# Optimization experiments

Measured on AMD Instinct MI355X. Metric: run time of the kernel, lower is better.

## Reference

```python
import jax, jax.numpy as jnp
import numpy as np

S = 7          # grid size
B = 2          # boxes per cell
C = 20         # classes (last dim = B*5 + C = 30)
IMG = 448.0    # img_size
GAMMA_COORD = 5.0
GAMMA_NOOBJ = 0.5
BS = 8192


def setup_inputs() -> dict:
    key = jax.random.key(0)
    k1, k2, k3 = jax.random.split(key, 3)
    output = jax.random.uniform(k1, (BS, S, S, B * 5 + C), dtype=jnp.float32)
    target = jax.random.uniform(k2, (BS, S, S, B * 5 + C), dtype=jnp.float32)
    grid_mask_obj = jax.random.randint(k3, (BS, S, S), 0, 2).astype(jnp.int32)
    return {"output": output, "target": target, "grid_mask_obj": grid_mask_obj}


def _decode_xyxy(t):
    """t: (bs,S,S,B*5) raw boxes -> pixel-space corner boxes x1,y1,x2,y2, each (bs,S,S,B)."""
    boxes = t.reshape(t.shape[:3] + (B, 5))
    cell = 1.0 / S
    gx = (jnp.arange(S, dtype=t.dtype) * cell)[None, None, :, None]  # varies along m (col)
    gy = (jnp.arange(S, dtype=t.dtype) * cell)[None, :, None, None]  # varies along n (row)
    x = (boxes[..., 0] * cell + gx) * IMG
    y = (boxes[..., 1] * cell + gy) * IMG
    w = boxes[..., 2] * IMG
    h = boxes[..., 3] * IMG
    return x - w / 2, y - h / 2, x + w / 2, y + h / 2


def _yolo_loss(output, target, grid_mask_obj):
    bs = output.shape[0]
    obj = (grid_mask_obj != 0).astype(output.dtype)          # (bs,S,S)

    boxes_o = output[..., : B * 5].reshape(output.shape[:3] + (B, 5))
    boxes_t = target[..., : B * 5].reshape(target.shape[:3] + (B, 5))

    # --- IoU of each predicted box vs target box 0 (matches box_iou(...)[:, 0]) ---
    ox1, oy1, ox2, oy2 = _decode_xyxy(output[..., : B * 5])   # (bs,S,S,B)
    tx1, ty1, tx2, ty2 = _decode_xyxy(target[..., : B * 5])
    tx1, ty1, tx2, ty2 = tx1[..., :1], ty1[..., :1], tx2[..., :1], ty2[..., :1]  # target box 0
    iw = jnp.clip(jnp.minimum(ox2, tx2) - jnp.maximum(ox1, tx1), 0.0)
    ih = jnp.clip(jnp.minimum(oy2, ty2) - jnp.maximum(oy1, ty1), 0.0)
    inter = iw * ih
    area_o = (ox2 - ox1) * (oy2 - oy1)
    area_t = (tx2 - tx1) * (ty2 - ty1)
    ious = inter / (area_o + area_t - inter)                  # (bs,S,S,B)

    max_iou = jnp.max(ious, axis=-1)                          # (bs,S,S)
    max_id = jnp.argmax(ious, axis=-1)                        # (bs,S,S)
    onehot = jax.nn.one_hot(max_id, B, dtype=output.dtype)
    obj_ij_mask = onehot * obj[..., None]
    obj_ij_ious = onehot * max_iou[..., None] * obj[..., None]

    box_id_reg = jnp.argmax(obj_ij_mask, axis=-1)             # (bs,S,S)
    box_id_conf = jnp.argmax(obj_ij_ious, axis=-1)

    sel_o = jnp.take_along_axis(boxes_o, box_id_reg[..., None, None], axis=3)[..., 0, :]
    sel_t = jnp.take_along_axis(boxes_t, box_id_reg[..., None, None], axis=3)[..., 0, :]
    xy_loss = jnp.sum(obj * jnp.sum((sel_o[..., 0:2] - sel_t[..., 0:2]) ** 2, axis=-1))
    wh_loss = jnp.sum(obj * jnp.sum((jnp.sqrt(sel_o[..., 2:4]) - jnp.sqrt(sel_t[..., 2:4])) ** 2, axis=-1))

    # --- confidence loss (obj cells): predicted conf vs matched IoU ---
    conf_o = boxes_o[..., 4]                                  # (bs,S,S,B)
    conf_t = boxes_t[..., 4]
    sel_c = jnp.take_along_axis(conf_o, box_id_conf[..., None], axis=3)[..., 0]
    sel_iou = jnp.take_along_axis(obj_ij_ious, box_id_conf[..., None], axis=3)[..., 0]
    c_loss_obj = jnp.sum(obj * (sel_c - sel_iou) ** 2)

    # --- confidence loss (noobj cells): all B boxes ---
    c_loss_noobj = jnp.sum((1.0 - obj)[..., None] * (conf_o - conf_t) ** 2)

    # --- class probability loss (obj cells) ---
    cls_loss = jnp.sum(obj[..., None] * (output[..., B * 5:] - target[..., B * 5:]) ** 2)

    return (GAMMA_COORD * (xy_loss + wh_loss)
            + c_loss_obj
            + GAMMA_NOOBJ * c_loss_noobj
            + cls_loss) / bs


def reference(output, target, grid_mask_obj):
    return _yolo_loss(output, target, grid_mask_obj)
```

## Files before the change

### kernel.cpp

```cpp
#include <hip/hip_runtime.h>


constexpr float CELLW_  = 1.0f / 7.0f;
constexpr float IMG_    = 448.0f;
constexpr float INV_BS_ = 1.0f / 8192.0f;
constexpr int   NCELL_  = 8192 * 7 * 7;
constexpr int   NBLK_   = NCELL_ / 256;

__global__ __launch_bounds__(256) void yolo_partial_kernel(
    const float* __restrict__ outp, const float* __restrict__ tgtp,
    const int* __restrict__ maskp, float* __restrict__ partial)
{
    __shared__ int   lmask[256];
    __shared__ float lo[256 * 11];
    __shared__ float lt[256 * 11];

    const int tid   = threadIdx.x;
    const int cell0 = blockIdx.x * 256;

    lmask[tid] = maskp[cell0 + tid];
    __syncthreads();

    const float2* po = reinterpret_cast<const float2*>(outp) + (size_t)cell0 * 15;
    const float2* pt = reinterpret_cast<const float2*>(tgtp) + (size_t)cell0 * 15;

    float acc = 0.0f;

    int c  = (2 * tid) / 30;
    int ch = (2 * tid) - c * 30;

#pragma unroll
    for (int k = 0; k < 15; ++k) {
        const int j = tid + 256 * k;
        float2 vo = po[j];
        float2 vt = pt[j];
        if (ch < 10) {
            lo[c * 11 + ch]     = vo.x;
            lo[c * 11 + ch + 1] = vo.y;
            lt[c * 11 + ch]     = vt.x;
            lt[c * 11 + ch + 1] = vt.y;
        } else {
            float dx = vo.x - vt.x;
            float dy = vo.y - vt.y;
            acc += lmask[c] ? (dx * dx + dy * dy) : 0.0f;
        }
        ch += 2; c += 17;
        if (ch >= 30) { ch -= 30; c += 1; }
    }
    __syncthreads();

    {
        const float* o = &lo[tid * 11];
        const float* t = &lt[tid * 11];
        const int    m = lmask[tid];

        const int rem = (cell0 + tid) % 49;
        const float gx = (float)(rem % 7) * CELLW_;
        const float gy = (float)(rem / 7) * CELLW_;

        const float tx = (t[0] * CELLW_ + gx) * IMG_;
        const float ty = (t[1] * CELLW_ + gy) * IMG_;
        const float tw = t[2] * IMG_, th = t[3] * IMG_;
        const float tx1 = tx - tw * 0.5f, tx2 = tx + tw * 0.5f;
        const float ty1 = ty - th * 0.5f, ty2 = ty + th * 0.5f;
        const float area_t = (tx2 - tx1) * (ty2 - ty1);

        float iou[2];
#pragma unroll
        for (int b = 0; b < 2; ++b) {
            float b0 = (b == 0) ? o[0] : o[5];
            float b1 = (b == 0) ? o[1] : o[6];
            float b2 = (b == 0) ? o[2] : o[7];
            float b3 = (b == 0) ? o[3] : o[8];
            float x = (b0 * CELLW_ + gx) * IMG_;
            float y = (b1 * CELLW_ + gy) * IMG_;
            float w = b2 * IMG_, h = b3 * IMG_;
            float x1 = x - w * 0.5f, x2 = x + w * 0.5f;
            float y1 = y - h * 0.5f, y2 = y + h * 0.5f;
            float iw = fmaxf(fminf(x2, tx2) - fmaxf(x1, tx1), 0.0f);
            float ih = fmaxf(fminf(y2, ty2) - fmaxf(y1, ty1), 0.0f);
            float inter = iw * ih;
            float area_o = (x2 - x1) * (y2 - y1);
            iou[b] = inter / (area_o + area_t - inter);
        }

        const int   max_id  = (iou[1] > iou[0]) ? 1 : 0;
        const float max_iou = fmaxf(iou[0], iou[1]);

        const float so0 = max_id ? o[5] : o[0];
        const float so1 = max_id ? o[6] : o[1];
        const float so2 = max_id ? o[7] : o[2];
        const float so3 = max_id ? o[8] : o[3];
        const float st0 = max_id ? t[5] : t[0];
        const float st1 = max_id ? t[6] : t[1];
        const float st2 = max_id ? t[7] : t[2];
        const float st3 = max_id ? t[8] : t[3];

        const float dxy0 = so0 - st0, dxy1 = so1 - st1;
        const float xy_loss = dxy0 * dxy0 + dxy1 * dxy1;

        const float dwh0 = sqrtf(so2) - sqrtf(st2);
        const float dwh1 = sqrtf(so3) - sqrtf(st3);
        const float wh_loss = dwh0 * dwh0 + dwh1 * dwh1;

        const int   id_conf = (max_iou > 0.0f) ? max_id : 0;
        const float sel_c   = id_conf ? o[9] : o[4];
        const float sel_iou = (id_conf == max_id) ? max_iou : 0.0f;
        const float dcf     = sel_c - sel_iou;
        const float c_obj   = dcf * dcf;

        const float dn0 = o[4] - t[4], dn1 = o[9] - t[9];
        const float c_noobj = dn0 * dn0 + dn1 * dn1;

        acc += m ? (5.0f * (xy_loss + wh_loss) + c_obj)
                 : (0.5f * c_noobj);
    }

#pragma unroll
    for (int off = 32; off > 0; off >>= 1)
        acc += __shfl_down(acc, off);

    __shared__ float wsum[4];
    const int lane = threadIdx.x & 63;
    const int wid  = threadIdx.x >> 6;
    if (lane == 0) wsum[wid] = acc;
    __syncthreads();
    if (threadIdx.x == 0)
        partial[blockIdx.x] = wsum[0] + wsum[1] + wsum[2] + wsum[3];
}

__global__ __launch_bounds__(256) void yolo_reduce_kernel(
    const float* __restrict__ partial, float* __restrict__ out)
{
    float a = 0.0f;
    for (int i = threadIdx.x; i < NBLK_; i += 256)
        a += partial[i];

#pragma unroll
    for (int off = 32; off > 0; off >>= 1)
        a += __shfl_down(a, off);

    __shared__ float wsum[4];
    const int lane = threadIdx.x & 63;
    const int wid  = threadIdx.x >> 6;
    if (lane == 0) wsum[wid] = a;
    __syncthreads();
    if (threadIdx.x == 0)
        out[0] = (wsum[0] + wsum[1] + wsum[2] + wsum[3]) * INV_BS_;
}

extern "C" void kernel_launch(void* const* d_in, const int* in_sizes, int n_in,
                              void* d_out, int out_size, void* d_ws, size_t ws_size,
                              hipStream_t stream) {
    const float* outp = (const float*)d_in[0];
    const float* tgtp = (const float*)d_in[1];
    const int*   mask = (const int*)d_in[2];
    float*       res  = (float*)d_out;
    float*       part = (float*)d_ws;

    const int ncell = in_sizes[2];
    const int blocks = ncell / 256;

    yolo_partial_kernel<<<blocks, 256, 0, stream>>>(outp, tgtp, mask, part);
    yolo_reduce_kernel<<<1, 256, 0, stream>>>(part, res);
}
```

Measured before the change: 122.4 us.

## Stream inputs as float4 grid-stride pass and gather box fields only for object cells

Replaces the shared-memory staging with a persistent grid-stride loop over float4 elements. Each element is weighted by its channel type and mask, which covers the class loss and the noobj confidence loss. A second pass per cell re-reads the first ten box fields from global memory only for object cells to compute IoU and the coordinate and confidence losses. This removes LDS traffic and barriers and uses a fixed 2048-block grid, at the cost of extra mask loads and partly uncoalesced re-reads of box data, which should mostly hit cache.

```diff
diff --git a/kernel.cpp b/kernel.cpp
--- a/kernel.cpp
+++ b/kernel.cpp
@@ -1,119 +1,127 @@
 #include <hip/hip_runtime.h>
 
 
+constexpr int   NCELL_  = 8192 * 7 * 7;
+constexpr int   NF4_    = NCELL_ * 30 / 4;
+constexpr int   TPB_    = 256;
+constexpr int   NBLK_   = 2048;
+constexpr int   NTH_    = TPB_ * NBLK_;
 constexpr float CELLW_  = 1.0f / 7.0f;
 constexpr float IMG_    = 448.0f;
 constexpr float INV_BS_ = 1.0f / 8192.0f;
-constexpr int   NCELL_  = 8192 * 7 * 7;
-constexpr int   NBLK_   = NCELL_ / 256;
 
-__global__ __launch_bounds__(256) void yolo_partial_kernel(
+__global__ __launch_bounds__(TPB_) void yolo_partial_kernel(
     const float* __restrict__ outp, const float* __restrict__ tgtp,
     const int* __restrict__ maskp, float* __restrict__ partial)
 {
-    __shared__ int   lmask[256];
-    __shared__ float lo[256 * 11];
-    __shared__ float lt[256 * 11];
-
-    const int tid   = threadIdx.x;
-    const int cell0 = blockIdx.x * 256;
-
-    lmask[tid] = maskp[cell0 + tid];
-    __syncthreads();
-
-    const float2* po = reinterpret_cast<const float2*>(outp) + (size_t)cell0 * 15;
-    const float2* pt = reinterpret_cast<const float2*>(tgtp) + (size_t)cell0 * 15;
-
+    const int gtid = blockIdx.x * TPB_ + threadIdx.x;
     float acc = 0.0f;
 
-    int c  = (2 * tid) / 30;
-    int ch = (2 * tid) - c * 30;
+    {
+        const float4* o4p = reinterpret_cast<const float4*>(outp);
+        const float4* t4p = reinterpret_cast<const float4*>(tgtp);
+
+        unsigned D    = 4u * (unsigned)gtid;
+        unsigned cell = D / 30u;
+        int      ch   = (int)(D - cell * 30u);
+
+        for (int i = gtid; i < NF4_; i += NTH_) {
+            float4 o4 = o4p[i];
+            float4 t4 = t4p[i];
+            int m0 = maskp[cell];
+            int m1 = maskp[(ch == 28) ? cell + 1u : cell];
+            float mf0 = m0 ? 1.0f : 0.0f;
+            float mf1 = m1 ? 1.0f : 0.0f;
 
 #pragma unroll
-    for (int k = 0; k < 15; ++k) {
-        const int j = tid + 256 * k;
-        float2 vo = po[j];
-        float2 vt = pt[j];
-        if (ch < 10) {
-            lo[c * 11 + ch]     = vo.x;
-            lo[c * 11 + ch + 1] = vo.y;
-            lt[c * 11 + ch]     = vt.x;
-            lt[c * 11 + ch + 1] = vt.y;
-        } else {
-            float dx = vo.x - vt.x;
-            float dy = vo.y - vt.y;
-            acc += lmask[c] ? (dx * dx + dy * dy) : 0.0f;
+            for (int j = 0; j < 4; ++j) {
+                int   chj   = ch + j;
+                bool  cross = (chj >= 30);
+                int   chv   = cross ? chj - 30 : chj;
+                float mf    = cross ? mf1 : mf0;
+                float w = (chv >= 10) ? mf
+                        : ((chv == 4) | (chv == 9)) ? 0.5f * (1.0f - mf)
+                        : 0.0f;
+                float ov = (j == 0) ? o4.x : (j == 1) ? o4.y : (j == 2) ? o4.z : o4.w;
+                float tv = (j == 0) ? t4.x : (j == 1) ? t4.y : (j == 2) ? t4.z : t4.w;
+                float d = ov - tv;
+                acc += w * d * d;
+            }
+
+            cell += 69905u; ch += 2;
+            if (ch >= 30) { ch -= 30; cell += 1u; }
         }
-        ch += 2; c += 17;
-        if (ch >= 30) { ch -= 30; c += 1; }
     }
-    __syncthreads();
 
-    {
-        const float* o = &lo[tid * 11];
-        const float* t = &lt[tid * 11];
-        const int    m = lmask[tid];
+    if (gtid < NCELL_) {
+        const int c = gtid;
+        const int m = maskp[c];
+        if (m) {
+            const float2* po = reinterpret_cast<const float2*>(outp) + (size_t)c * 15;
+            const float2* pt = reinterpret_cast<const float2*>(tgtp) + (size_t)c * 15;
+            float2 a0 = po[0], a1 = po[1], a2 = po[2], a3 = po[3], a4 = po[4];
+            float2 b0 = pt[0], b1 = pt[1], b2 = pt[2], b3 = pt[3], b4 = pt[4];
+            const float o0 = a0.x, o1 = a0.y, o2 = a1.x, o3 = a1.y, o4v = a2.x;
+            const float o5 = a2.y, o6 = a3.x, o7 = a3.y, o8 = a4.x, o9 = a4.y;
+            const float t0 = b0.x, t1 = b0.y, t2 = b1.x, t3 = b1.y;
+            const float t5 = b2.y, t6 = b3.x, t7 = b3.y, t8 = b4.x;
 
-        const int rem = (cell0 + tid) % 49;
-        const float gx = (float)(rem % 7) * CELLW_;
-        const float gy = (float)(rem / 7) * CELLW_;
+            const int rem = c % 49;
+            const float gx = (float)(rem % 7) * CELLW_;
+            const float gy = (float)(rem / 7) * CELLW_;
 
-        const float tx = (t[0] * CELLW_ + gx) * IMG_;
-        const float ty = (t[1] * CELLW_ + gy) * IMG_;
-        const float tw = t[2] * IMG_, th = t[3] * IMG_;
-        const float tx1 = tx - tw * 0.5f, tx2 = tx + tw * 0.5f;
-        const float ty1 = ty - th * 0.5f, ty2 = ty + th * 0.5f;
-        const float area_t = (tx2 - tx1) * (ty2 - ty1);
+            const float tx = (t0 * CELLW_ + gx) * IMG_;
+            const float ty = (t1 * CELLW_ + gy) * IMG_;
+            const float tw = t2 * IMG_, th = t3 * IMG_;
+            const float tx1 = tx - tw * 0.5f, tx2 = tx + tw * 0.5f;
+            const float ty1 = ty - th * 0.5f, ty2 = ty + th * 0.5f;
+            const float area_t = (tx2 - tx1) * (ty2 - ty1);
 
-        float iou[2];
+            float iou[2];
 #pragma unroll
-        for (int b = 0; b < 2; ++b) {
-            float b0 = (b == 0) ? o[0] : o[5];
-            float b1 = (b == 0) ? o[1] : o[6];
-            float b2 = (b == 0) ? o[2] : o[7];
-            float b3 = (b == 0) ? o[3] : o[8];
-            float x = (b0 * CELLW_ + gx) * IMG_;
-            float y = (b1 * CELLW_ + gy) * IMG_;
-            float w = b2 * IMG_, h = b3 * IMG_;
-            float x1 = x - w * 0.5f, x2 = x + w * 0.5f;
-            float y1 = y - h * 0.5f, y2 = y + h * 0.5f;
-            float iw = fmaxf(fminf(x2, tx2) - fmaxf(x1, tx1), 0.0f);
-            float ih = fmaxf(fminf(y2, ty2) - fmaxf(y1, ty1), 0.0f);
-            float inter = iw * ih;
-            float area_o = (x2 - x1) * (y2 - y1);
-            iou[b] = inter / (area_o + area_t - inter);
+            for (int b = 0; b < 2; ++b) {
+                float bx = (b == 0) ? o0 : o5;
+                float by = (b == 0) ? o1 : o6;
+                float bw = (b == 0) ? o2 : o7;
+                float bh = (b == 0) ? o3 : o8;
+                float x = (bx * CELLW_ + gx) * IMG_;
+                float y = (by * CELLW_ + gy) * IMG_;
+                float w = bw * IMG_, h = bh * IMG_;
+                float x1 = x - w * 0.5f, x2 = x + w * 0.5f;
+                float y1 = y - h * 0.5f, y2 = y + h * 0.5f;
+                float iw = fmaxf(fminf(x2, tx2) - fmaxf(x1, tx1), 0.0f);
+                float ih = fmaxf(fminf(y2, ty2) - fmaxf(y1, ty1), 0.0f);
+                float inter = iw * ih;
+                float area_o = (x2 - x1) * (y2 - y1);
+                iou[b] = inter / (area_o + area_t - inter);
+            }
+
+            const int   max_id  = (iou[1] > iou[0]) ? 1 : 0;
+            const float max_iou = fmaxf(iou[0], iou[1]);
+
+            const float so0 = max_id ? o5 : o0;
+            const float so1 = max_id ? o6 : o1;
+            const float so2 = max_id ? o7 : o2;
+            const float so3 = max_id ? o8 : o3;
+            const float st0 = max_id ? t5 : t0;
+            const float st1 = max_id ? t6 : t1;
+            const float st2 = max_id ? t7 : t2;
+            const float st3 = max_id ? t8 : t3;
+
+            const float dxy0 = so0 - st0, dxy1 = so1 - st1;
+            const float xy_loss = dxy0 * dxy0 + dxy1 * dxy1;
+
+            const float dwh0 = sqrtf(so2) - sqrtf(st2);
+            const float dwh1 = sqrtf(so3) - sqrtf(st3);
+            const float wh_loss = dwh0 * dwh0 + dwh1 * dwh1;
+
+            const int   id_conf = (max_iou > 0.0f) ? max_id : 0;
+            const float sel_c   = id_conf ? o9 : o4v;
+            const float sel_iou = (id_conf == max_id) ? max_iou : 0.0f;
+            const float dcf     = sel_c - sel_iou;
+
+            acc += 5.0f * (xy_loss + wh_loss) + dcf * dcf;
         }
-
-        const int   max_id  = (iou[1] > iou[0]) ? 1 : 0;
-        const float max_iou = fmaxf(iou[0], iou[1]);
-
-        const float so0 = max_id ? o[5] : o[0];
-        const float so1 = max_id ? o[6] : o[1];
-        const float so2 = max_id ? o[7] : o[2];
-        const float so3 = max_id ? o[8] : o[3];
-        const float st0 = max_id ? t[5] : t[0];
-        const float st1 = max_id ? t[6] : t[1];
-        const float st2 = max_id ? t[7] : t[2];
-        const float st3 = max_id ? t[8] : t[3];
-
-        const float dxy0 = so0 - st0, dxy1 = so1 - st1;
-        const float xy_loss = dxy0 * dxy0 + dxy1 * dxy1;
-
-        const float dwh0 = sqrtf(so2) - sqrtf(st2);
-        const float dwh1 = sqrtf(so3) - sqrtf(st3);
-        const float wh_loss = dwh0 * dwh0 + dwh1 * dwh1;
-
-        const int   id_conf = (max_iou > 0.0f) ? max_id : 0;
-        const float sel_c   = id_conf ? o[9] : o[4];
-        const float sel_iou = (id_conf == max_id) ? max_iou : 0.0f;
-        const float dcf     = sel_c - sel_iou;
-        const float c_obj   = dcf * dcf;
-
-        const float dn0 = o[4] - t[4], dn1 = o[9] - t[9];
-        const float c_noobj = dn0 * dn0 + dn1 * dn1;
-
-        acc += m ? (5.0f * (xy_loss + wh_loss) + c_obj)
-                 : (0.5f * c_noobj);
     }
 
 #pragma unroll
@@ -158,9 +166,6 @@
     float*       res  = (float*)d_out;
     float*       part = (float*)d_ws;
 
-    const int ncell = in_sizes[2];
-    const int blocks = ncell / 256;
-
-    yolo_partial_kernel<<<blocks, 256, 0, stream>>>(outp, tgtp, mask, part);
+    yolo_partial_kernel<<<NBLK_, TPB_, 0, stream>>>(outp, tgtp, mask, part);
     yolo_reduce_kernel<<<1, 256, 0, stream>>>(part, res);
 }
```

Result: no change. 121.8 us (-0.5%).
